# Performance work log

Measured on AMD Instinct MI355X. Metric: run time of the kernel, lower is better.

The kernel has to match this reference:

```python
import jax, jax.numpy as jnp
import numpy as np

P, NL, NQ, L, P2L, P2Q, D = 50000, 2000, 6000, 8, 128, 64, 32
MAX_MODELS, NPOL, MAXQ, ITERS = 7, 4, 3, 8
ZS = {'traffic': (1385.4059, 859.8119), 'packets': (1.4015, 0.8933), 'eq_lambda': (1350.9712, 858.3162), 'avg_pkts_lambda': (0.9117, 0.9724), 'exp_max_factor': (6.6636, 4.7151), 'pkts_lambda_on': (0.9116, 1.6513), 'avg_t_off': (1.6649, 2.3564), 'avg_t_on': (1.6649, 2.3564), 'ar_a': (0.0, 1.0), 'sigma': (0.0, 1.0), 'capacity': (27611.0918, 20090.6211), 'queue_size': (30259.1055, 21410.0957)}


def _glorot(k, fin, fout):
    lim = float(np.sqrt(6.0 / (fin + fout)))
    return jax.random.uniform(k, (fin, fout), jnp.float32, -lim, lim)


def setup_inputs():
    keys = iter(jax.random.split(jax.random.key(0), 80))
    nk = lambda: next(keys)
    u = lambda shape, lo=0.0, hi=1.0: jax.random.uniform(nk(), shape, jnp.float32, lo, hi)
    inp = {}
    inp['traffic'] = u((P, 1), 1.0, 3000.0)
    inp['packets'] = u((P, 1), 0.5, 3.0)
    inp['eq_lambda'] = u((P, 1), 1.0, 3000.0)
    inp['avg_pkts_lambda'] = u((P, 1))
    inp['exp_max_factor'] = u((P, 1), 1.0, 12.0)
    inp['pkts_lambda_on'] = u((P, 1))
    inp['avg_t_off'] = u((P, 1), 0.1, 4.0)
    inp['avg_t_on'] = u((P, 1), 0.1, 4.0)
    inp['ar_a'] = jax.random.normal(nk(), (P, 1), jnp.float32)
    inp['sigma'] = jax.random.normal(nk(), (P, 1), jnp.float32)
    inp['capacity'] = u((NL, 1), 8000.0, 60000.0)
    inp['queue_size'] = u((NQ, 1), 1000.0, 64000.0)
    inp['weight'] = u((NQ, 1))
    length = jax.random.randint(nk(), (P,), 1, L + 1)
    inp['length'] = length
    inp['model'] = jax.random.randint(nk(), (P,), 0, MAX_MODELS)
    inp['policy'] = jax.random.randint(nk(), (NL,), 0, NPOL)
    inp['priority'] = jax.random.randint(nk(), (NQ,), 0, MAXQ)
    inp['queue_to_path'] = jax.random.randint(nk(), (P, L), 0, NQ)
    inp['link_to_path'] = jax.random.randint(nk(), (P, L), 0, NL)
    p2l_path = jax.random.randint(nk(), (NL, P2L), 0, P)
    inp['path_to_link'] = jnp.stack([p2l_path, jnp.zeros_like(p2l_path)], -1)
    inp['p2l_deg'] = jax.random.randint(nk(), (NL,), 1, P2L + 1)
    pq_path = jax.random.randint(nk(), (NQ, P2Q), 0, P)
    pq_pos = 1 + jax.random.randint(nk(), (NQ, P2Q), 0, L) % length[pq_path]
    inp['path_to_queue'] = jnp.stack([pq_path, pq_pos], -1)
    inp['p2q_deg'] = jax.random.randint(nk(), (NQ,), 1, P2Q + 1)
    inp['queue_to_link'] = jnp.arange(NL * MAXQ).reshape(NL, MAXQ)
    def dense(fin, fout):
        return _glorot(nk(), fin, fout), jnp.zeros((fout,), jnp.float32)
    inp['pe_w1'], inp['pe_b1'] = dense(10 + MAX_MODELS, D)
    inp['pe_w2'], inp['pe_b2'] = dense(D, D)
    inp['le_w1'], inp['le_b1'] = dense(NPOL + 1, D)
    inp['le_w2'], inp['le_b2'] = dense(D, D)
    inp['qe_w1'], inp['qe_b1'] = dense(MAXQ + 2, D)
    inp['qe_w2'], inp['qe_b2'] = dense(D, D)
    inp['prW'] = _glorot(nk(), 2 * D, D); inp['prU'] = _glorot(nk(), D, D); inp['prB'] = jnp.zeros((D,), jnp.float32)
    inp['qrW'] = _glorot(nk(), D, D); inp['qrU'] = _glorot(nk(), D, D); inp['qrB'] = jnp.zeros((D,), jnp.float32)
    inp['lrW'] = _glorot(nk(), D, D); inp['lrU'] = _glorot(nk(), D, D); inp['lrB'] = jnp.zeros((D,), jnp.float32)
    inp['ro_w1'], inp['ro_b1'] = dense(D, D // 2)
    inp['ro_w2'], inp['ro_b2'] = dense(D // 2, D // 2)
    inp['ro_w3'], inp['ro_b3'] = dense(D // 2, 1)
    return inp


def _mlp2(x, w1, b1, w2, b2):
    return jax.nn.relu(jax.nn.relu(x @ w1 + b1) @ w2 + b2)


def _forward(traffic, packets, eq_lambda, avg_pkts_lambda, exp_max_factor, pkts_lambda_on,
             avg_t_off, avg_t_on, ar_a, sigma, capacity, queue_size, weight,
             pe_w1, pe_b1, pe_w2, pe_b2, le_w1, le_b1, le_w2, le_b2, qe_w1, qe_b1, qe_w2, qe_b2,
             prW, prU, prB, qrW, qrU, qrB, lrW, lrU, lrB,
             ro_w1, ro_b1, ro_w2, ro_b2, ro_w3, ro_b3,
             length, model, policy, priority, queue_to_path, link_to_path,
             path_to_link, path_to_queue, queue_to_link, p2l_deg, p2q_deg):
    dt = traffic.dtype
    nz = lambda x, k: (x - ZS[k][0]) / ZS[k][1]
    # link load: masked ragged sum of traffic of paths crossing each link
    p2l_mask = (jnp.arange(P2L) < p2l_deg[:, None]).astype(dt)                # [NL, P2L]
    path_gather_traffic = traffic[path_to_link[:, :, 0], 0]                   # [NL, P2L]
    load = (path_gather_traffic * p2l_mask).sum(1, keepdims=True) / capacity  # [NL, 1]
    pkt_size = traffic / packets                                              # [P, 1]
    path_features = jnp.concatenate([
        nz(traffic, 'traffic'), nz(packets, 'packets'),
        jax.nn.one_hot(model, MAX_MODELS, dtype=dt),
        nz(eq_lambda, 'eq_lambda'), nz(avg_pkts_lambda, 'avg_pkts_lambda'),
        nz(exp_max_factor, 'exp_max_factor'), nz(pkts_lambda_on, 'pkts_lambda_on'),
        nz(avg_t_off, 'avg_t_off'), nz(avg_t_on, 'avg_t_on'),
        nz(ar_a, 'ar_a'), nz(sigma, 'sigma')], axis=1)                         # [P, 17]
    path_state = _mlp2(path_features, pe_w1, pe_b1, pe_w2, pe_b2)             # [P, D]
    link_state = _mlp2(jnp.concatenate([load, jax.nn.one_hot(policy, NPOL, dtype=dt)], 1),
                       le_w1, le_b1, le_w2, le_b2)                             # [NL, D]
    queue_state = _mlp2(jnp.concatenate([nz(queue_size, 'queue_size'),
                                         jax.nn.one_hot(priority, MAXQ, dtype=dt), weight], 1),
                        qe_w1, qe_b1, qe_w2, qe_b2)                            # [NQ, D]
    hop_mask = (jnp.arange(L) < length[:, None]).astype(dt)                    # [P, L]
    p2q_mask = (jnp.arange(P2Q) < p2q_deg[:, None]).astype(dt)                 # [NQ, P2Q]

    def path_step(h, xs):
        x_t, m_t = xs
        h_new = jnp.tanh(x_t @ prW + h @ prU + prB)
        h = m_t[:, None] * h_new + (1.0 - m_t[:, None]) * h  # ragged: freeze past length
        return h, h

    pss = None
    for _ in range(ITERS):
        qg = queue_state[queue_to_path]                                        # [P, L, D]
        lg = link_state[link_to_path]                                          # [P, L, D]
        xin = jnp.concatenate([qg, lg], -1)                                    # [P, L, 2D]
        prev = path_state
        path_state, seq = jax.lax.scan(path_step, path_state,
                                       (jnp.swapaxes(xin, 0, 1), hop_mask.T))
        pss = jnp.concatenate([prev[:, None], jnp.swapaxes(seq, 0, 1)], 1)     # [P, L+1, D]
        pg = pss[path_to_queue[:, :, 0], path_to_queue[:, :, 1]]               # [NQ, P2Q, D]
        path_sum = (pg * p2q_mask[:, :, None]).sum(1)                          # [NQ, D]
        queue_state = jnp.tanh(path_sum @ qrW + queue_state @ qrU + qrB)
        qgl = queue_state[queue_to_link]                                       # [NL, 3, D]
        h = link_state
        for t in range(MAXQ):  # fixed tiny sequence of 3 queues per link
            h = jnp.tanh(qgl[:, t] @ lrW + h @ lrU + lrB)
        link_state = h
    cap_g = capacity[link_to_path, 0]                                          # [P, L]
    occ = jax.nn.relu(pss[:, 1:] @ ro_w1 + ro_b1)
    occ = jax.nn.relu(occ @ ro_w2 + ro_b2)
    occ = (occ @ ro_w3 + ro_b3)[:, :, 0]                                       # [P, L]
    queue_delay = ((occ / cap_g) * hop_mask).sum(1, keepdims=True)             # [P, 1]
    trans_delay = pkt_size * ((1.0 / cap_g) * hop_mask).sum(1, keepdims=True)  # [P, 1]
    return queue_delay + trans_delay


def reference(traffic, packets, eq_lambda, avg_pkts_lambda, exp_max_factor, pkts_lambda_on,
              avg_t_off, avg_t_on, ar_a, sigma, capacity, queue_size, weight,
              pe_w1, pe_b1, pe_w2, pe_b2, le_w1, le_b1, le_w2, le_b2, qe_w1, qe_b1, qe_w2, qe_b2,
              prW, prU, prB, qrW, qrU, qrB, lrW, lrU, lrB,
              ro_w1, ro_b1, ro_w2, ro_b2, ro_w3, ro_b3,
              length, model, policy, priority, queue_to_path, link_to_path,
              path_to_link, path_to_queue, queue_to_link, p2l_deg, p2q_deg):
    return _forward(traffic, packets, eq_lambda, avg_pkts_lambda, exp_max_factor, pkts_lambda_on,
                    avg_t_off, avg_t_on, ar_a, sigma, capacity, queue_size, weight,
                    pe_w1, pe_b1, pe_w2, pe_b2, le_w1, le_b1, le_w2, le_b2, qe_w1, qe_b1, qe_w2, qe_b2,
                    prW, prU, prB, qrW, qrU, qrB, lrW, lrU, lrB,
                    ro_w1, ro_b1, ro_w2, ro_b2, ro_w3, ro_b3,
                    length, model, policy, priority, queue_to_path, link_to_path,
                    path_to_link, path_to_queue, queue_to_link, p2l_deg, p2q_deg)
```

## Files before the change

kernel.cpp:

```cpp
#include <hip/hip_runtime.h>
#include <hip/hip_bf16.h>

#define P_ 50000
#define NL_ 2000
#define NQ_ 6000
#define L_ 8
#define P2L_ 128
#define P2Q_ 64
#define D_ 32
#define ITERS_ 8

typedef __hip_bfloat16 bf16;
typedef unsigned short u16;
typedef unsigned int u32;

__device__ __forceinline__ float bfb2f(u16 u) {
    union { u32 i; float f; } c; c.i = ((u32)u) << 16; return c.f;
}
__device__ __forceinline__ u16 f2bfb(float f) {
    union { bf16 h; u16 u; } c; c.h = __float2bfloat16(f); return c.u;
}
__device__ __forceinline__ u32 pk2(float a, float b) {
    return (u32)f2bfb(a) | ((u32)f2bfb(b) << 16);
}

__device__ __forceinline__ float tanh_fast(float x) {
    return 1.f - 2.f / (__expf(2.f * x) + 1.f);
}

__device__ __forceinline__ void hr_rebuild(float* hr, float4 own) {
    hr[0] = own.x; hr[1] = own.y; hr[2] = own.z; hr[3] = own.w;
#pragma unroll
    for (int c = 0; c < 4; c++)  hr[4 + c]  = __shfl_xor(hr[c], 1, 64);
#pragma unroll
    for (int c = 0; c < 8; c++)  hr[8 + c]  = __shfl_xor(hr[c], 2, 64);
#pragma unroll
    for (int c = 0; c < 16; c++) hr[16 + c] = __shfl_xor(hr[c], 4, 64);
}

__device__ __forceinline__ float4 matvec32(const float* hr,
                                           const float* const* ub, float4 acc) {
#pragma unroll
    for (int s = 0; s < 8; s++) {
#pragma unroll
        for (int c = 0; c < 4; c++) {
            const float4 u = *(const float4*)(ub[s] + 32 * c);
            const float hk = hr[4 * s + c];
            acc.x += hk * u.x; acc.y += hk * u.y;
            acc.z += hk * u.z; acc.w += hk * u.w;
        }
    }
    return acc;
}

__device__ bool detect_f32(const void* p, int n) {
    const u16* u = (const u16*)p;
    int m = n < 64 ? n : 64;
    bool bad = false;
    for (int k = 0; k < m; k++) {
        float v = bfb2f(u[k]);
        float av = fabsf(v);
        bool sane = (v == v) && (av <= 1e6f) && (av == 0.0f || av >= 1e-8f);
        bad |= !sane;
    }
    return bad;
}


struct CvtArgs { const void* p[40]; };

__global__ __launch_bounds__(256) void k_convert(CvtArgs a, float* __restrict__ dst) {
    static constexpr int N[40] = {
        50000,50000,50000,50000,50000,50000,50000,50000,50000,50000,
        2000,6000,6000,
        544,32,1024,32, 160,32,1024,32, 160,32,1024,32,
        2048,1024,32, 1024,1024,32, 1024,1024,32,
        512,16,256,16,16,1};
    int b = blockIdx.x, t = 0, off = 0;
    for (;;) {
        int nb = (N[t] + 255) >> 8;
        if (b < nb) break;
        b -= nb; off += N[t]; ++t;
    }
    const void* src = a.p[t];
    const int n = N[t];
    const bool isf = detect_f32(src, n);
    const int i = b * 256 + threadIdx.x;
    if (i < n)
        dst[off + i] = isf ? ((const float*)src)[i] : bfb2f(((const u16*)src)[i]);
}


__global__ __launch_bounds__(256) void k_path_embed(
    const float* __restrict__ traffic, const float* __restrict__ packets,
    const float* __restrict__ eq_lambda, const float* __restrict__ avg_pkts_lambda,
    const float* __restrict__ exp_max_factor, const float* __restrict__ pkts_lambda_on,
    const float* __restrict__ avg_t_off, const float* __restrict__ avg_t_on,
    const float* __restrict__ ar_a, const float* __restrict__ sigma,
    const int* __restrict__ model,
    const float* __restrict__ w1, const float* __restrict__ b1,
    const float* __restrict__ w2, const float* __restrict__ b2,
    float* __restrict__ path_state)
{
    int p = blockIdx.x * 256 + threadIdx.x;
    if (p >= P_) return;
    float f[10];
    f[0] = (traffic[p]        - 1385.4059f) * (1.f / 859.8119f);
    f[1] = (packets[p]        - 1.4015f)    * (1.f / 0.8933f);
    f[2] = (eq_lambda[p]      - 1350.9712f) * (1.f / 858.3162f);
    f[3] = (avg_pkts_lambda[p]- 0.9117f)    * (1.f / 0.9724f);
    f[4] = (exp_max_factor[p] - 6.6636f)    * (1.f / 4.7151f);
    f[5] = (pkts_lambda_on[p] - 0.9116f)    * (1.f / 1.6513f);
    f[6] = (avg_t_off[p]      - 1.6649f)    * (1.f / 2.3564f);
    f[7] = (avg_t_on[p]       - 1.6649f)    * (1.f / 2.3564f);
    f[8] = ar_a[p];
    f[9] = sigma[p];
    int mrow = 2 + model[p];
    float h1[32];
#pragma unroll
    for (int d = 0; d < 32; d++) {
        float a = b1[d] + w1[mrow * 32 + d];
        a += f[0] * w1[0 * 32 + d];
        a += f[1] * w1[1 * 32 + d];
#pragma unroll
        for (int j = 0; j < 8; j++) a += f[2 + j] * w1[(9 + j) * 32 + d];
        h1[d] = fmaxf(a, 0.f);
    }
#pragma unroll
    for (int d = 0; d < 32; d++) {
        float a = b2[d];
#pragma unroll
        for (int k = 0; k < 32; k++) a += h1[k] * w2[k * 32 + d];
        path_state[p * 32 + d] = fmaxf(a, 0.f);
    }
}

__global__ __launch_bounds__(256) void k_queue_embed(
    const float* __restrict__ queue_size, const float* __restrict__ weight,
    const int* __restrict__ priority,
    const float* __restrict__ w1, const float* __restrict__ b1,
    const float* __restrict__ w2, const float* __restrict__ b2,
    float* __restrict__ queue_state)
{
    int q = blockIdx.x * 256 + threadIdx.x;
    if (q >= NQ_) return;
    float f0 = (queue_size[q] - 30259.1055f) * (1.f / 21410.0957f);
    float f4 = weight[q];
    int prow = 1 + priority[q];
    float h1[32];
#pragma unroll
    for (int d = 0; d < 32; d++) {
        float a = b1[d] + w1[prow * 32 + d]
                + f0 * w1[0 * 32 + d] + f4 * w1[4 * 32 + d];
        h1[d] = fmaxf(a, 0.f);
    }
#pragma unroll
    for (int d = 0; d < 32; d++) {
        float a = b2[d];
#pragma unroll
        for (int k = 0; k < 32; k++) a += h1[k] * w2[k * 32 + d];
        queue_state[q * 32 + d] = fmaxf(a, 0.f);
    }
}

__global__ __launch_bounds__(256) void k_link_embed(
    const float* __restrict__ traffic, const float* __restrict__ capacity,
    const int* __restrict__ policy,
    const int* __restrict__ p2l, const int* __restrict__ p2l_deg,
    const float* __restrict__ w1, const float* __restrict__ b1,
    const float* __restrict__ w2, const float* __restrict__ b2,
    float* __restrict__ link_state)
{
    __shared__ float wsh[1248];
    __shared__ float h1s[4][32];
    const int tid = threadIdx.x;
    if (tid < 160) wsh[tid] = w1[tid];
    if (tid < 32)  wsh[160 + tid] = b1[tid];
    for (int idx = tid; idx < 1024; idx += 256) wsh[192 + idx] = w2[idx];
    if (tid >= 32 && tid < 64) wsh[1216 + tid - 32] = b2[tid - 32];
    __syncthreads();

    const int w = tid >> 6, lane = tid & 63;
    const int l = blockIdx.x * 4 + w;
    const int deg = p2l_deg[l];
    float s = 0.f;
    if (lane < deg)      s += traffic[p2l[l * 256 + 2 * lane]];
    if (lane + 64 < deg) s += traffic[p2l[l * 256 + 2 * (lane + 64)]];
#pragma unroll
    for (int m = 1; m < 64; m <<= 1) s += __shfl_xor(s, m, 64);
    const float load = s / capacity[l];
    const int prow = 1 + policy[l];
    if (lane < 32) {
        float a = wsh[160 + lane] + wsh[prow * 32 + lane] + load * wsh[lane];
        h1s[w][lane] = fmaxf(a, 0.f);
    }
    __syncthreads();
    if (lane < 32) {
        float a = wsh[1216 + lane];
#pragma unroll
        for (int k = 0; k < 32; k++) a += h1s[w][k] * wsh[192 + k * 32 + lane];
        link_state[l * 32 + lane] = fmaxf(a, 0.f);
    }
}


__global__ __launch_bounds__(256) void k_zprep(
    const float* __restrict__ queue_state, const float* __restrict__ link_state,
    const float* __restrict__ prW, const float* __restrict__ prB,
    float* __restrict__ zq, float* __restrict__ zl)
{
    __shared__ float wq[32 * 32];
    __shared__ float wlk[32 * 32];
    __shared__ float bsh[32];
    const int tid = threadIdx.x;
#pragma unroll
    for (int j = 0; j < 4; j++) {
        wq[tid + 256 * j]  = prW[tid + 256 * j];
        wlk[tid + 256 * j] = prW[1024 + tid + 256 * j];
    }
    if (tid < 32) bsh[tid] = prB[tid];
    __syncthreads();

    const int grp = tid >> 3, i = tid & 7;
    const int e = blockIdx.x * 32 + grp;
    if (e >= NQ_ + NL_) return;
    const bool isq = e < NQ_;
    const float* st = isq ? (queue_state + (size_t)e * 32)
                          : (link_state + (size_t)(e - NQ_) * 32);
    const float* wbase = isq ? wq : wlk;
    const float* ub[8];
#pragma unroll
    for (int s = 0; s < 8; s++) ub[s] = wbase + (i ^ s) * 128 + 4 * i;

    float4 own = *(const float4*)(st + 4 * i);
    float hr[32];
    hr_rebuild(hr, own);

    float4 acc;
    if (isq) acc = *(const float4*)(bsh + 4 * i);
    else     acc = make_float4(0.f, 0.f, 0.f, 0.f);
    acc = matvec32(hr, ub, acc);

    float* dst = isq ? (zq + (size_t)e * 32) : (zl + (size_t)(e - NQ_) * 32);
    *(float4*)(dst + 4 * i) = acc;
}


__global__ __launch_bounds__(256, 2) void k_path_rnn(
    const int* __restrict__ q2p, const int* __restrict__ l2p,
    const int* __restrict__ length,
    const float* __restrict__ prU,
    const float* __restrict__ zq, const float* __restrict__ zl,
    float* __restrict__ path_state, u16* __restrict__ pss)
{
    const int tid = threadIdx.x;
    const int grp = tid >> 3, i = tid & 7;
    const int p = blockIdx.x * 32 + grp;
    if (p >= P_) return;
    const int len = length[p];

    float4 Ub[32];
#pragma unroll
    for (int s = 0; s < 8; s++) {
        const float* rb = prU + ((i ^ s) * 128 + 4 * i);
#pragma unroll
        for (int c = 0; c < 4; c++)
            Ub[4 * s + c] = *(const float4*)(rb + 32 * c);
    }

    const int4 qi0 = *(const int4*)(q2p + (size_t)p * 8);
    const int4 qi1 = *(const int4*)(q2p + (size_t)p * 8 + 4);
    const int4 li0 = *(const int4*)(l2p + (size_t)p * 8);
    const int4 li1 = *(const int4*)(l2p + (size_t)p * 8 + 4);
    const int qidx[8] = {qi0.x, qi0.y, qi0.z, qi0.w, qi1.x, qi1.y, qi1.z, qi1.w};
    const int lidx[8] = {li0.x, li0.y, li0.z, li0.w, li1.x, li1.y, li1.z, li1.w};

    float4 own = *(const float4*)(path_state + (size_t)p * 32 + 4 * i);
    float hr[32];
    hr_rebuild(hr, own);

    float4 z;
    {
        const float4 a = *(const float4*)(zq + (size_t)qidx[0] * 32 + 4 * i);
        const float4 b = *(const float4*)(zl + (size_t)lidx[0] * 32 + 4 * i);
        z = make_float4(a.x + b.x, a.y + b.y, a.z + b.z, a.w + b.w);
    }

#pragma unroll
    for (int t = 0; t < 8; t++) {
        float4 acc = z;
        if (t < 7) {
            const float4 a = *(const float4*)(zq + (size_t)qidx[t + 1] * 32 + 4 * i);
            const float4 b = *(const float4*)(zl + (size_t)lidx[t + 1] * 32 + 4 * i);
            z = make_float4(a.x + b.x, a.y + b.y, a.z + b.z, a.w + b.w);
        }
#pragma unroll
        for (int k = 0; k < 32; k++) {
            const float hk = hr[k];
            acc.x += hk * Ub[k].x; acc.y += hk * Ub[k].y;
            acc.z += hk * Ub[k].z; acc.w += hk * Ub[k].w;
        }
        const bool m = (t < len);
        own.x = m ? tanh_fast(acc.x) : own.x;
        own.y = m ? tanh_fast(acc.y) : own.y;
        own.z = m ? tanh_fast(acc.z) : own.z;
        own.w = m ? tanh_fast(acc.w) : own.w;
        uint2 w2;
        w2.x = pk2(own.x, own.y);
        w2.y = pk2(own.z, own.w);
        *(uint2*)(pss + (size_t)p * 256 + t * 32 + 4 * i) = w2;
        if (t < 7) hr_rebuild(hr, own);
    }
    *(float4*)(path_state + (size_t)p * 32 + 4 * i) = own;
}


__global__ __launch_bounds__(256) void k_queue_update(
    const int* __restrict__ p2q, const int* __restrict__ p2q_deg,
    const float* __restrict__ qrW, const float* __restrict__ qrU,
    const float* __restrict__ qrB,
    const float* __restrict__ prWq, const float* __restrict__ prB,
    const u16* __restrict__ pss, float* __restrict__ queue_state,
    float* __restrict__ zq)
{
    __shared__ float wl[3 * 1024 + 64];
    const int tid = threadIdx.x;
#pragma unroll
    for (int j = 0; j < 4; j++) {
        wl[tid + 256 * j]        = qrW[tid + 256 * j];
        wl[1024 + tid + 256 * j] = qrU[tid + 256 * j];
        wl[2048 + tid + 256 * j] = prWq[tid + 256 * j];
    }
    if (tid < 32) { wl[3072 + tid] = qrB[tid]; wl[3104 + tid] = prB[tid]; }
    __syncthreads();

    const int w = tid >> 6, lane = tid & 63;
    const int g = lane >> 3, i = lane & 7;
    const int q = blockIdx.x * 4 + w;
    const int deg = p2q_deg[q];

    float4 ps = {0.f, 0.f, 0.f, 0.f};
    for (int j = g; j < deg; j += 8) {
        const int pj = p2q[q * 128 + 2 * j];
        int pos = p2q[q * 128 + 2 * j + 1] - 1;
        pos = pos < 0 ? 0 : (pos > 7 ? 7 : pos);
        const ushort4 v = *(const ushort4*)(pss + (size_t)pj * 256 + pos * 32 + 4 * i);
        ps.x += bfb2f(v.x); ps.y += bfb2f(v.y);
        ps.z += bfb2f(v.z); ps.w += bfb2f(v.w);
    }
#pragma unroll
    for (int m = 8; m < 64; m <<= 1) {
        ps.x += __shfl_xor(ps.x, m, 64);
        ps.y += __shfl_xor(ps.y, m, 64);
        ps.z += __shfl_xor(ps.z, m, 64);
        ps.w += __shfl_xor(ps.w, m, 64);
    }
    const float4 qs = *(const float4*)(queue_state + (size_t)q * 32 + 4 * i);

    const float* ubW[8]; const float* ubU[8]; const float* ubP[8];
#pragma unroll
    for (int s = 0; s < 8; s++) {
        const int o = (i ^ s) * 128 + 4 * i;
        ubW[s] = wl + o; ubU[s] = wl + 1024 + o; ubP[s] = wl + 2048 + o;
    }

    float psr[32]; hr_rebuild(psr, ps);
    float qsr[32]; hr_rebuild(qsr, qs);
    float4 acc = *(const float4*)(wl + 3072 + 4 * i);
    acc = matvec32(psr, ubW, acc);
    acc = matvec32(qsr, ubU, acc);
    float4 nh;
    nh.x = tanh_fast(acc.x); nh.y = tanh_fast(acc.y);
    nh.z = tanh_fast(acc.z); nh.w = tanh_fast(acc.w);

    float nhr[32]; hr_rebuild(nhr, nh);
    float4 zacc = *(const float4*)(wl + 3104 + 4 * i);
    zacc = matvec32(nhr, ubP, zacc);

    if (g == 0) {
        *(float4*)(queue_state + (size_t)q * 32 + 4 * i) = nh;
        *(float4*)(zq + (size_t)q * 32 + 4 * i) = zacc;
    }
}


__global__ __launch_bounds__(256) void k_link_update(
    const int* __restrict__ q2l,
    const float* __restrict__ lrW, const float* __restrict__ lrU,
    const float* __restrict__ lrB,
    const float* __restrict__ prWl,
    const float* __restrict__ queue_state, float* __restrict__ link_state,
    float* __restrict__ zl)
{
    __shared__ float wl[3 * 1024 + 32];
    const int tid = threadIdx.x;
#pragma unroll
    for (int j = 0; j < 4; j++) {
        wl[tid + 256 * j]        = lrW[tid + 256 * j];
        wl[1024 + tid + 256 * j] = lrU[tid + 256 * j];
        wl[2048 + tid + 256 * j] = prWl[tid + 256 * j];
    }
    if (tid < 32) wl[3072 + tid] = lrB[tid];
    __syncthreads();

    const int w = tid >> 6, lane = tid & 63;
    const int i = lane & 7, g = lane >> 3;
    const int l = blockIdx.x * 4 + w;

    const float* ubW[8]; const float* ubU[8]; const float* ubP[8];
#pragma unroll
    for (int s = 0; s < 8; s++) {
        const int o = (i ^ s) * 128 + 4 * i;
        ubW[s] = wl + o; ubU[s] = wl + 1024 + o; ubP[s] = wl + 2048 + o;
    }

    float4 h = *(const float4*)(link_state + (size_t)l * 32 + 4 * i);
    float hhr[32]; hr_rebuild(hhr, h);

#pragma unroll
    for (int t = 0; t < 3; t++) {
        const int qq = q2l[l * 3 + t];
        const float4 qg = *(const float4*)(queue_state + (size_t)qq * 32 + 4 * i);
        float qgr[32]; hr_rebuild(qgr, qg);
        float4 acc = *(const float4*)(wl + 3072 + 4 * i);
        acc = matvec32(qgr, ubW, acc);
        acc = matvec32(hhr, ubU, acc);
        h.x = tanh_fast(acc.x); h.y = tanh_fast(acc.y);
        h.z = tanh_fast(acc.z); h.w = tanh_fast(acc.w);
        hr_rebuild(hhr, h);
    }
    float4 zacc = make_float4(0.f, 0.f, 0.f, 0.f);
    zacc = matvec32(hhr, ubP, zacc);

    if (g == 0) {
        *(float4*)(link_state + (size_t)l * 32 + 4 * i) = h;
        *(float4*)(zl + (size_t)l * 32 + 4 * i) = zacc;
    }
}


__global__ __launch_bounds__(256) void k_readout(
    const void* __restrict__ raw_traffic,
    const float* __restrict__ traffic, const float* __restrict__ packets,
    const float* __restrict__ capacity,
    const int* __restrict__ l2p, const int* __restrict__ length,
    const float* __restrict__ w1, const float* __restrict__ b1,
    const float* __restrict__ w2, const float* __restrict__ b2,
    const float* __restrict__ w3, const float* __restrict__ b3,
    const u16* __restrict__ pss, void* __restrict__ out)
{
    __shared__ float wl[817];
    __shared__ float xs[32][52];
    const int tid = threadIdx.x;
    for (int idx = tid; idx < 512; idx += 256) wl[idx] = w1[idx];
    if (tid < 256) wl[528 + tid] = w2[tid];
    if (tid < 16) {
        wl[512 + tid] = b1[tid];
        wl[784 + tid] = b2[tid];
        wl[800 + tid] = w3[tid];
    }
    if (tid == 0) wl[816] = b3[0];
    __syncthreads();

    const int grp = tid >> 3, i = tid & 7;
    const int p = blockIdx.x * 32 + grp;
    if (p >= P_) return;
    const bool outf32 = detect_f32(raw_traffic, P_);
    const int len = length[p];
    float qd = 0.f, ts = 0.f;
#pragma unroll 1
    for (int t = 0; t < 8; t++) {
        const ushort4 hu = *(const ushort4*)(pss + (size_t)p * 256 + t * 32 + 4 * i);
        float4 hv;
        hv.x = bfb2f(hu.x); hv.y = bfb2f(hu.y); hv.z = bfb2f(hu.z); hv.w = bfb2f(hu.w);
        *(float4*)&xs[grp][4 * i] = hv;
        float a0 = wl[512 + 2 * i], a1 = wl[512 + 2 * i + 1];
#pragma unroll
        for (int k = 0; k < 32; k += 4) {
            const float4 xv = *(const float4*)&xs[grp][k];
            const float2 u0 = *(const float2*)&wl[(k + 0) * 16 + 2 * i];
            const float2 u1 = *(const float2*)&wl[(k + 1) * 16 + 2 * i];
            const float2 u2 = *(const float2*)&wl[(k + 2) * 16 + 2 * i];
            const float2 u3 = *(const float2*)&wl[(k + 3) * 16 + 2 * i];
            a0 += xv.x * u0.x + xv.y * u1.x + xv.z * u2.x + xv.w * u3.x;
            a1 += xv.x * u0.y + xv.y * u1.y + xv.z * u2.y + xv.w * u3.y;
        }
        a0 = fmaxf(a0, 0.f); a1 = fmaxf(a1, 0.f);
        *(float2*)&xs[grp][32 + 2 * i] = make_float2(a0, a1);
        float c0 = wl[784 + 2 * i], c1 = wl[784 + 2 * i + 1];
#pragma unroll
        for (int k = 0; k < 16; k += 4) {
            const float4 xv = *(const float4*)&xs[grp][32 + k];
            const float2 u0 = *(const float2*)&wl[528 + (k + 0) * 16 + 2 * i];
            const float2 u1 = *(const float2*)&wl[528 + (k + 1) * 16 + 2 * i];
            const float2 u2 = *(const float2*)&wl[528 + (k + 2) * 16 + 2 * i];
            const float2 u3 = *(const float2*)&wl[528 + (k + 3) * 16 + 2 * i];
            c0 += xv.x * u0.x + xv.y * u1.x + xv.z * u2.x + xv.w * u3.x;
            c1 += xv.x * u0.y + xv.y * u1.y + xv.z * u2.y + xv.w * u3.y;
        }
        c0 = fmaxf(c0, 0.f); c1 = fmaxf(c1, 0.f);
        float pv = c0 * wl[800 + 2 * i] + c1 * wl[800 + 2 * i + 1];
        pv += __shfl_xor(pv, 1, 8);
        pv += __shfl_xor(pv, 2, 8);
        pv += __shfl_xor(pv, 4, 8);
        const float occv = pv + wl[816];
        if (t < len) {
            const float inv = 1.f / capacity[l2p[p * 8 + t]];
            qd += occv * inv;
            ts += inv;
        }
    }
    if (i == 0) {
        const float res = qd + (traffic[p] / packets[p]) * ts;
        if (outf32) ((float*)out)[p] = res;
        else        ((bf16*)out)[p] = __float2bfloat16(res);
    }
}


extern "C" void kernel_launch(void* const* d_in, const int* in_sizes, int n_in,
                              void* d_out, int out_size, void* d_ws, size_t ws_size,
                              hipStream_t stream)
{
    static const int CVT_N[40] = {
        50000,50000,50000,50000,50000,50000,50000,50000,50000,50000,
        2000,6000,6000,
        544,32,1024,32, 160,32,1024,32, 160,32,1024,32,
        2048,1024,32, 1024,1024,32, 1024,1024,32,
        512,16,256,16,16,1};

    const int*  length   = (const int*)d_in[13];
    const int*  model    = (const int*)d_in[14];
    const int*  policy   = (const int*)d_in[15];
// ... 32 lines not shown
    const float* c_pe_w1 = ws + off[13]; const float* c_pe_b1 = ws + off[14];
    const float* c_pe_w2 = ws + off[15]; const float* c_pe_b2 = ws + off[16];
    const float* c_le_w1 = ws + off[17]; const float* c_le_b1 = ws + off[18];
    const float* c_le_w2 = ws + off[19]; const float* c_le_b2 = ws + off[20];
    const float* c_qe_w1 = ws + off[21]; const float* c_qe_b1 = ws + off[22];
    const float* c_qe_w2 = ws + off[23]; const float* c_qe_b2 = ws + off[24];
    const float* c_prW = ws + off[25]; const float* c_prU = ws + off[26];
    const float* c_prB = ws + off[27];
    const float* c_qrW = ws + off[28]; const float* c_qrU = ws + off[29];
    const float* c_qrB = ws + off[30];
    const float* c_lrW = ws + off[31]; const float* c_lrU = ws + off[32];
    const float* c_lrB = ws + off[33];
    const float* c_ro_w1 = ws + off[34]; const float* c_ro_b1 = ws + off[35];
    const float* c_ro_w2 = ws + off[36]; const float* c_ro_b2 = ws + off[37];
    const float* c_ro_w3 = ws + off[38]; const float* c_ro_b3 = ws + off[39];

    size_t base = ((size_t)off[40] + 63) & ~(size_t)63;
    float* path_state  = ws + base;
    float* queue_state = path_state + (size_t)P_ * 32;
    float* link_state  = queue_state + (size_t)NQ_ * 32;
    float* zq          = link_state + (size_t)NL_ * 32;
    float* zl          = zq + (size_t)NQ_ * 32;
    u16*   pss         = (u16*)(zl + (size_t)NL_ * 32);

    k_convert<<<nblk, 256, 0, stream>>>(ca, ws);

    k_path_embed<<<(P_ + 255) / 256, 256, 0, stream>>>(
        c_traffic, c_packets, c_eq_lambda, c_apl, c_emf, c_plo, c_atoff, c_aton,
        c_ar_a, c_sigma, model, c_pe_w1, c_pe_b1, c_pe_w2, c_pe_b2, path_state);
    k_queue_embed<<<(NQ_ + 255) / 256, 256, 0, stream>>>(
        c_queue_size, c_weight, priority, c_qe_w1, c_qe_b1, c_qe_w2, c_qe_b2,
        queue_state);
    k_link_embed<<<NL_ / 4, 256, 0, stream>>>(
        c_traffic, c_capacity, policy, p2l, p2l_deg,
        c_le_w1, c_le_b1, c_le_w2, c_le_b2, link_state);
    k_zprep<<<(NQ_ + NL_ + 31) / 32, 256, 0, stream>>>(
        queue_state, link_state, c_prW, c_prB, zq, zl);

    for (int it = 0; it < ITERS_; ++it) {
        k_path_rnn<<<(P_ + 31) / 32, 256, 0, stream>>>(
            q2p, l2p, length, c_prU, zq, zl, path_state, pss);
        k_queue_update<<<NQ_ / 4, 256, 0, stream>>>(
            p2q, p2q_deg, c_qrW, c_qrU, c_qrB, c_prW, c_prB,
            pss, queue_state, zq);
        k_link_update<<<NL_ / 4, 256, 0, stream>>>(
            q2l, c_lrW, c_lrU, c_lrB, c_prW + 1024,
            queue_state, link_state, zl);
    }

    k_readout<<<(P_ + 31) / 32, 256, 0, stream>>>(
        d_in[0], c_traffic, c_packets, c_capacity, l2p, length,
        c_ro_w1, c_ro_b1, c_ro_w2, c_ro_b2, c_ro_w3, c_ro_b3, pss, d_out);
}
```

Before: 724.7 us.

## Sort paths by length, skip padded RNN steps, fuse embed and update kernels

```diff
diff --git a/kernel.cpp b/kernel.cpp
--- a/kernel.cpp
+++ b/kernel.cpp
@@ -9,6 +9,8 @@
 #define P2Q_ 64
 #define D_ 32
 #define ITERS_ 8
+#define PB_ 196
+#define QB_ 24
 
 typedef __hip_bfloat16 bf16;
 typedef unsigned short u16;
@@ -27,6 +29,9 @@
 __device__ __forceinline__ float tanh_fast(float x) {
     return 1.f - 2.f / (__expf(2.f * x) + 1.f);
 }
+__device__ __forceinline__ float4 tanh4(float4 a) {
+    return make_float4(tanh_fast(a.x), tanh_fast(a.y), tanh_fast(a.z), tanh_fast(a.w));
+}
 
 __device__ __forceinline__ void hr_rebuild(float* hr, float4 own) {
     hr[0] = own.x; hr[1] = own.y; hr[2] = own.z; hr[3] = own.w;
@@ -38,13 +43,14 @@
     for (int c = 0; c < 16; c++) hr[16 + c] = __shfl_xor(hr[c], 4, 64);
 }
 
-__device__ __forceinline__ float4 matvec32(const float* hr,
-                                           const float* const* ub, float4 acc) {
+__device__ __forceinline__ float4 matvec32o(const float* hr, const float* base,
+                                            const int* offs, float4 acc) {
 #pragma unroll
     for (int s = 0; s < 8; s++) {
+        const float* u0 = base + offs[s];
 #pragma unroll
         for (int c = 0; c < 4; c++) {
-            const float4 u = *(const float4*)(ub[s] + 32 * c);
+            const float4 u = *(const float4*)(u0 + 32 * c);
             const float hk = hr[4 * s + c];
             acc.x += hk * u.x; acc.y += hk * u.y;
             acc.z += hk * u.z; acc.w += hk * u.w;
@@ -69,13 +75,15 @@
 
 struct CvtArgs { const void* p[40]; };
 
-__global__ __launch_bounds__(256) void k_convert(CvtArgs a, float* __restrict__ dst) {
+__global__ __launch_bounds__(256) void k_convert(CvtArgs a, float* __restrict__ dst,
+                                                 int* __restrict__ counters) {
     static constexpr int N[40] = {
         50000,50000,50000,50000,50000,50000,50000,50000,50000,50000,
         2000,6000,6000,
         544,32,1024,32, 160,32,1024,32, 160,32,1024,32,
         2048,1024,32, 1024,1024,32, 1024,1024,32,
         512,16,256,16,16,1};
+    if (blockIdx.x == 0 && threadIdx.x < 16) counters[threadIdx.x] = 0;
     int b = blockIdx.x, t = 0, off = 0;
     for (;;) {
         int nb = (N[t] + 255) >> 8;
@@ -91,162 +99,157 @@
 }
 
 
-__global__ __launch_bounds__(256) void k_path_embed(
+__global__ __launch_bounds__(256) void k_hist(const int* __restrict__ length,
+                                              int* __restrict__ hist) {
+    int p = blockIdx.x * 256 + threadIdx.x;
+    if (p < P_) atomicAdd(&hist[length[p] - 1], 1);
+}
+
+__global__ __launch_bounds__(256) void k_scatter(const int* __restrict__ length,
+                                                 const int* __restrict__ hist,
+                                                 int* __restrict__ cursor,
+                                                 int* __restrict__ perm) {
+    int p = blockIdx.x * 256 + threadIdx.x;
+    if (p >= P_) return;
+    int b = length[p] - 1;
+    int pre = 0;
+#pragma unroll
+    for (int k = 0; k < 8; k++) pre += (k < b) ? hist[k] : 0;
+    int pos = pre + atomicAdd(&cursor[b], 1);
+    perm[pos] = p;
+}
+
+
+__global__ __launch_bounds__(256) void k_embed_all(
     const float* __restrict__ traffic, const float* __restrict__ packets,
     const float* __restrict__ eq_lambda, const float* __restrict__ avg_pkts_lambda,
     const float* __restrict__ exp_max_factor, const float* __restrict__ pkts_lambda_on,
     const float* __restrict__ avg_t_off, const float* __restrict__ avg_t_on,
     const float* __restrict__ ar_a, const float* __restrict__ sigma,
-    const int* __restrict__ model,
-    const float* __restrict__ w1, const float* __restrict__ b1,
-    const float* __restrict__ w2, const float* __restrict__ b2,
-    float* __restrict__ path_state)
+    const float* __restrict__ capacity, const float* __restrict__ queue_size,
+    const float* __restrict__ weight,
+    const int* __restrict__ model, const int* __restrict__ policy,
+    const int* __restrict__ priority,
+    const int* __restrict__ p2l, const int* __restrict__ p2l_deg,
+    const float* __restrict__ pe_w1, const float* __restrict__ pe_b1,
+    const float* __restrict__ pe_w2, const float* __restrict__ pe_b2,
+    const float* __restrict__ qe_w1, const float* __restrict__ qe_b1,
+    const float* __restrict__ qe_w2, const float* __restrict__ qe_b2,
+    const float* __restrict__ le_w1, const float* __restrict__ le_b1,
+    const float* __restrict__ le_w2, const float* __restrict__ le_b2,
+    const float* __restrict__ prW, const float* __restrict__ prB,
+    float* __restrict__ path_state, float* __restrict__ queue_state,
+    float* __restrict__ link_state, float* __restrict__ zq, float* __restrict__ zl)
 {
-    int p = blockIdx.x * 256 + threadIdx.x;
-    if (p >= P_) return;
-    float f[10];
-    f[0] = (traffic[p]        - 1385.4059f) * (1.f / 859.8119f);
-    f[1] = (packets[p]        - 1.4015f)    * (1.f / 0.8933f);
-    f[2] = (eq_lambda[p]      - 1350.9712f) * (1.f / 858.3162f);
-    f[3] = (avg_pkts_lambda[p]- 0.9117f)    * (1.f / 0.9724f);
-    f[4] = (exp_max_factor[p] - 6.6636f)    * (1.f / 4.7151f);
-    f[5] = (pkts_lambda_on[p] - 0.9116f)    * (1.f / 1.6513f);
-    f[6] = (avg_t_off[p]      - 1.6649f)    * (1.f / 2.3564f);
-    f[7] = (avg_t_on[p]       - 1.6649f)    * (1.f / 2.3564f);
-    f[8] = ar_a[p];
-    f[9] = sigma[p];
-    int mrow = 2 + model[p];
-    float h1[32];
-#pragma unroll
-    for (int d = 0; d < 32; d++) {
-        float a = b1[d] + w1[mrow * 32 + d];
-        a += f[0] * w1[0 * 32 + d];
-        a += f[1] * w1[1 * 32 + d];
-#pragma unroll
-        for (int j = 0; j < 8; j++) a += f[2 + j] * w1[(9 + j) * 32 + d];
-        h1[d] = fmaxf(a, 0.f);
-    }
-#pragma unroll
-    for (int d = 0; d < 32; d++) {
-        float a = b2[d];
-#pragma unroll
-        for (int k = 0; k < 32; k++) a += h1[k] * w2[k * 32 + d];
-        path_state[p * 32 + d] = fmaxf(a, 0.f);
-    }
-}
-
-__global__ __launch_bounds__(256) void k_queue_embed(
-    const float* __restrict__ queue_size, const float* __restrict__ weight,
-    const int* __restrict__ priority,
-    const float* __restrict__ w1, const float* __restrict__ b1,
-    const float* __restrict__ w2, const float* __restrict__ b2,
-    float* __restrict__ queue_state)
-{
-    int q = blockIdx.x * 256 + threadIdx.x;
-    if (q >= NQ_) return;
-    float f0 = (queue_size[q] - 30259.1055f) * (1.f / 21410.0957f);
-    float f4 = weight[q];
-    int prow = 1 + priority[q];
-    float h1[32];
-#pragma unroll
-    for (int d = 0; d < 32; d++) {
-        float a = b1[d] + w1[prow * 32 + d]
-                + f0 * w1[0 * 32 + d] + f4 * w1[4 * 32 + d];
-        h1[d] = fmaxf(a, 0.f);
-    }
-#pragma unroll
-    for (int d = 0; d < 32; d++) {
-        float a = b2[d];
-#pragma unroll
-        for (int k = 0; k < 32; k++) a += h1[k] * w2[k * 32 + d];
-        queue_state[q * 32 + d] = fmaxf(a, 0.f);
-    }
-}
-
-__global__ __launch_bounds__(256) void k_link_embed(
-    const float* __restrict__ traffic, const float* __restrict__ capacity,
-    const int* __restrict__ policy,
-    const int* __restrict__ p2l, const int* __restrict__ p2l_deg,
-    const float* __restrict__ w1, const float* __restrict__ b1,
-    const float* __restrict__ w2, const float* __restrict__ b2,
-    float* __restrict__ link_state)
-{
-    __shared__ float wsh[1248];
-    __shared__ float h1s[4][32];
-    const int tid = threadIdx.x;
-    if (tid < 160) wsh[tid] = w1[tid];
-    if (tid < 32)  wsh[160 + tid] = b1[tid];
-    for (int idx = tid; idx < 1024; idx += 256) wsh[192 + idx] = w2[idx];
-    if (tid >= 32 && tid < 64) wsh[1216 + tid - 32] = b2[tid - 32];
-    __syncthreads();
-
-    const int w = tid >> 6, lane = tid & 63;
-    const int l = blockIdx.x * 4 + w;
-    const int deg = p2l_deg[l];
-    float s = 0.f;
-    if (lane < deg)      s += traffic[p2l[l * 256 + 2 * lane]];
-    if (lane + 64 < deg) s += traffic[p2l[l * 256 + 2 * (lane + 64)]];
-#pragma unroll
-    for (int m = 1; m < 64; m <<= 1) s += __shfl_xor(s, m, 64);
-    const float load = s / capacity[l];
-    const int prow = 1 + policy[l];
-    if (lane < 32) {
-        float a = wsh[160 + lane] + wsh[prow * 32 + lane] + load * wsh[lane];
-        h1s[w][lane] = fmaxf(a, 0.f);
-    }
-    __syncthreads();
-    if (lane < 32) {
-        float a = wsh[1216 + lane];
-#pragma unroll
-        for (int k = 0; k < 32; k++) a += h1s[w][k] * wsh[192 + k * 32 + lane];
-        link_state[l * 32 + lane] = fmaxf(a, 0.f);
-    }
-}
-
-
-__global__ __launch_bounds__(256) void k_zprep(
-    const float* __restrict__ queue_state, const float* __restrict__ link_state,
-    const float* __restrict__ prW, const float* __restrict__ prB,
-    float* __restrict__ zq, float* __restrict__ zl)
-{
-    __shared__ float wq[32 * 32];
-    __shared__ float wlk[32 * 32];
-    __shared__ float bsh[32];
-    const int tid = threadIdx.x;
-#pragma unroll
-    for (int j = 0; j < 4; j++) {
-        wq[tid + 256 * j]  = prW[tid + 256 * j];
-        wlk[tid + 256 * j] = prW[1024 + tid + 256 * j];
-    }
-    if (tid < 32) bsh[tid] = prB[tid];
-    __syncthreads();
-
-    const int grp = tid >> 3, i = tid & 7;
-    const int e = blockIdx.x * 32 + grp;
-    if (e >= NQ_ + NL_) return;
-    const bool isq = e < NQ_;
-    const float* st = isq ? (queue_state + (size_t)e * 32)
-                          : (link_state + (size_t)(e - NQ_) * 32);
-    const float* wbase = isq ? wq : wlk;
-    const float* ub[8];
-#pragma unroll
-    for (int s = 0; s < 8; s++) ub[s] = wbase + (i ^ s) * 128 + 4 * i;
-
-    float4 own = *(const float4*)(st + 4 * i);
-    float hr[32];
-    hr_rebuild(hr, own);
-
-    float4 acc;
-    if (isq) acc = *(const float4*)(bsh + 4 * i);
-    else     acc = make_float4(0.f, 0.f, 0.f, 0.f);
-    acc = matvec32(hr, ub, acc);
-
-    float* dst = isq ? (zq + (size_t)e * 32) : (zl + (size_t)(e - NQ_) * 32);
-    *(float4*)(dst + 4 * i) = acc;
+    const int blk = blockIdx.x;
+    if (blk < PB_) {
+        int p = blk * 256 + threadIdx.x;
+        if (p >= P_) return;
+        float f[10];
+        f[0] = (traffic[p]        - 1385.4059f) * (1.f / 859.8119f);
+        f[1] = (packets[p]        - 1.4015f)    * (1.f / 0.8933f);
+        f[2] = (eq_lambda[p]      - 1350.9712f) * (1.f / 858.3162f);
+        f[3] = (avg_pkts_lambda[p]- 0.9117f)    * (1.f / 0.9724f);
+        f[4] = (exp_max_factor[p] - 6.6636f)    * (1.f / 4.7151f);
+        f[5] = (pkts_lambda_on[p] - 0.9116f)    * (1.f / 1.6513f);
+        f[6] = (avg_t_off[p]      - 1.6649f)    * (1.f / 2.3564f);
+        f[7] = (avg_t_on[p]       - 1.6649f)    * (1.f / 2.3564f);
+        f[8] = ar_a[p];
+        f[9] = sigma[p];
+        int mrow = 2 + model[p];
+        float h1[32];
+#pragma unroll
+        for (int d = 0; d < 32; d++) {
+            float a = pe_b1[d] + pe_w1[mrow * 32 + d];
+            a += f[0] * pe_w1[0 * 32 + d];
+            a += f[1] * pe_w1[1 * 32 + d];
+#pragma unroll
+            for (int j = 0; j < 8; j++) a += f[2 + j] * pe_w1[(9 + j) * 32 + d];
+            h1[d] = fmaxf(a, 0.f);
+        }
+#pragma unroll
+        for (int d = 0; d < 32; d++) {
+            float a = pe_b2[d];
+#pragma unroll
+            for (int k = 0; k < 32; k++) a += h1[k] * pe_w2[k * 32 + d];
+            path_state[p * 32 + d] = fmaxf(a, 0.f);
+        }
+    } else if (blk < PB_ + QB_) {
+        int q = (blk - PB_) * 256 + threadIdx.x;
+        if (q >= NQ_) return;
+        float f0 = (queue_size[q] - 30259.1055f) * (1.f / 21410.0957f);
+        float f4 = weight[q];
+        int prow = 1 + priority[q];
+        float h1[32];
+#pragma unroll
+        for (int d = 0; d < 32; d++) {
+            float a = qe_b1[d] + qe_w1[prow * 32 + d]
+                    + f0 * qe_w1[0 * 32 + d] + f4 * qe_w1[4 * 32 + d];
+            h1[d] = fmaxf(a, 0.f);
+        }
+        float h2[32];
+#pragma unroll
+        for (int d = 0; d < 32; d++) {
+            float a = qe_b2[d];
+#pragma unroll
+            for (int k = 0; k < 32; k++) a += h1[k] * qe_w2[k * 32 + d];
+            h2[d] = fmaxf(a, 0.f);
+            queue_state[q * 32 + d] = h2[d];
+        }
+#pragma unroll
+        for (int d = 0; d < 32; d++) {
+            float a = prB[d];
+#pragma unroll
+            for (int k = 0; k < 32; k++) a += h2[k] * prW[k * 32 + d];
+            zq[q * 32 + d] = a;
+        }
+    } else {
+        __shared__ float wsh[1248];
+        __shared__ float h1s[4][32];
+        __shared__ float h2s[4][32];
+        const int tid = threadIdx.x;
+        if (tid < 160) wsh[tid] = le_w1[tid];
+        if (tid < 32)  wsh[160 + tid] = le_b1[tid];
+        for (int idx = tid; idx < 1024; idx += 256) wsh[192 + idx] = le_w2[idx];
+        if (tid >= 32 && tid < 64) wsh[1216 + tid - 32] = le_b2[tid - 32];
+        __syncthreads();
+
+        const int w = tid >> 6, lane = tid & 63;
+        const int l = (blk - PB_ - QB_) * 4 + w;
+        const int deg = p2l_deg[l];
+        float s = 0.f;
+        if (lane < deg)      s += traffic[p2l[l * 256 + 2 * lane]];
+        if (lane + 64 < deg) s += traffic[p2l[l * 256 + 2 * (lane + 64)]];
+#pragma unroll
+        for (int m = 1; m < 64; m <<= 1) s += __shfl_xor(s, m, 64);
+        const float load = s / capacity[l];
+        const int prow = 1 + policy[l];
+        if (lane < 32) {
+            float a = wsh[160 + lane] + wsh[prow * 32 + lane] + load * wsh[lane];
+            h1s[w][lane] = fmaxf(a, 0.f);
+        }
+        __syncthreads();
+        if (lane < 32) {
+            float a = wsh[1216 + lane];
+#pragma unroll
+            for (int k = 0; k < 32; k++) a += h1s[w][k] * wsh[192 + k * 32 + lane];
+            a = fmaxf(a, 0.f);
+            link_state[l * 32 + lane] = a;
+            h2s[w][lane] = a;
+        }
+        __syncthreads();
+        if (lane < 32) {
+            float a = 0.f;
+#pragma unroll
+            for (int k = 0; k < 32; k++) a += h2s[w][k] * prW[1024 + k * 32 + lane];
+            zl[l * 32 + lane] = a;
+        }
+    }
 }
 
 
 __global__ __launch_bounds__(256, 2) void k_path_rnn(
+    const int* __restrict__ perm,
     const int* __restrict__ q2p, const int* __restrict__ l2p,
     const int* __restrict__ length,
     const float* __restrict__ prU,
@@ -255,8 +258,9 @@
 {
     const int tid = threadIdx.x;
     const int grp = tid >> 3, i = tid & 7;
-    const int p = blockIdx.x * 32 + grp;
-    if (p >= P_) return;
+    const int j = blockIdx.x * 32 + grp;
+    if (j >= P_) return;
+    const int p = perm[j];
     const int len = length[p];
 
     float4 Ub[32];
@@ -267,31 +271,25 @@
         for (int c = 0; c < 4; c++)
             Ub[4 * s + c] = *(const float4*)(rb + 32 * c);
     }
-
-    const int4 qi0 = *(const int4*)(q2p + (size_t)p * 8);
-    const int4 qi1 = *(const int4*)(q2p + (size_t)p * 8 + 4);
-    const int4 li0 = *(const int4*)(l2p + (size_t)p * 8);
-    const int4 li1 = *(const int4*)(l2p + (size_t)p * 8 + 4);
-    const int qidx[8] = {qi0.x, qi0.y, qi0.z, qi0.w, qi1.x, qi1.y, qi1.z, qi1.w};
-    const int lidx[8] = {li0.x, li0.y, li0.z, li0.w, li1.x, li1.y, li1.z, li1.w};
 
     float4 own = *(const float4*)(path_state + (size_t)p * 32 + 4 * i);
     float hr[32];
     hr_rebuild(hr, own);
 
+    int qn = q2p[p * 8], ln = l2p[p * 8];
     float4 z;
     {
-        const float4 a = *(const float4*)(zq + (size_t)qidx[0] * 32 + 4 * i);
-        const float4 b = *(const float4*)(zl + (size_t)lidx[0] * 32 + 4 * i);
+        const float4 a = *(const float4*)(zq + (size_t)qn * 32 + 4 * i);
+        const float4 b = *(const float4*)(zl + (size_t)ln * 32 + 4 * i);
         z = make_float4(a.x + b.x, a.y + b.y, a.z + b.z, a.w + b.w);
     }
 
-#pragma unroll
-    for (int t = 0; t < 8; t++) {
+    for (int t = 0; t < len; t++) {
         float4 acc = z;
-        if (t < 7) {
-            const float4 a = *(const float4*)(zq + (size_t)qidx[t + 1] * 32 + 4 * i);
-            const float4 b = *(const float4*)(zl + (size_t)lidx[t + 1] * 32 + 4 * i);
+        if (t + 1 < len) {
+            qn = q2p[p * 8 + t + 1]; ln = l2p[p * 8 + t + 1];
+            const float4 a = *(const float4*)(zq + (size_t)qn * 32 + 4 * i);
+            const float4 b = *(const float4*)(zl + (size_t)ln * 32 + 4 * i);
             z = make_float4(a.x + b.x, a.y + b.y, a.z + b.z, a.w + b.w);
         }
 #pragma unroll
@@ -300,138 +298,107 @@
             acc.x += hk * Ub[k].x; acc.y += hk * Ub[k].y;
             acc.z += hk * Ub[k].z; acc.w += hk * Ub[k].w;
         }
-        const bool m = (t < len);
-        own.x = m ? tanh_fast(acc.x) : own.x;
-        own.y = m ? tanh_fast(acc.y) : own.y;
-        own.z = m ? tanh_fast(acc.z) : own.z;
-        own.w = m ? tanh_fast(acc.w) : own.w;
+        own = tanh4(acc);
         uint2 w2;
         w2.x = pk2(own.x, own.y);
         w2.y = pk2(own.z, own.w);
         *(uint2*)(pss + (size_t)p * 256 + t * 32 + 4 * i) = w2;
-        if (t < 7) hr_rebuild(hr, own);
+        if (t + 1 < len) hr_rebuild(hr, own);
     }
     *(float4*)(path_state + (size_t)p * 32 + 4 * i) = own;
 }
 
 
-__global__ __launch_bounds__(256) void k_queue_update(
+__global__ __launch_bounds__(256) void k_qlupd(
     const int* __restrict__ p2q, const int* __restrict__ p2q_deg,
+    const int* __restrict__ q2l,
     const float* __restrict__ qrW, const float* __restrict__ qrU,
     const float* __restrict__ qrB,
-    const float* __restrict__ prWq, const float* __restrict__ prB,
+    const float* __restrict__ lrW, const float* __restrict__ lrU,
+    const float* __restrict__ lrB,
+    const float* __restrict__ prW, const float* __restrict__ prB,
     const u16* __restrict__ pss, float* __restrict__ queue_state,
-    float* __restrict__ zq)
+    float* __restrict__ link_state,
+    float* __restrict__ zq, float* __restrict__ zl)
 {
-    __shared__ float wl[3 * 1024 + 64];
+    __shared__ float wl[6 * 1024 + 96];
     const int tid = threadIdx.x;
 #pragma unroll
-    for (int j = 0; j < 4; j++) {
-        wl[tid + 256 * j]        = qrW[tid + 256 * j];
-        wl[1024 + tid + 256 * j] = qrU[tid + 256 * j];
-        wl[2048 + tid + 256 * j] = prWq[tid + 256 * j];
-    }
-    if (tid < 32) { wl[3072 + tid] = qrB[tid]; wl[3104 + tid] = prB[tid]; }
+    for (int jj = 0; jj < 4; jj++) {
+        wl[tid + 256 * jj]        = qrW[tid + 256 * jj];
+        wl[1024 + tid + 256 * jj] = qrU[tid + 256 * jj];
+        wl[2048 + tid + 256 * jj] = prW[tid + 256 * jj];
+        wl[3072 + tid + 256 * jj] = lrW[tid + 256 * jj];
+        wl[4096 + tid + 256 * jj] = lrU[tid + 256 * jj];
+        wl[5120 + tid + 256 * jj] = prW[1024 + tid + 256 * jj];
+    }
+    if (tid < 32) {
+        wl[6144 + tid] = qrB[tid];
+        wl[6176 + tid] = prB[tid];
+        wl[6208 + tid] = lrB[tid];
+    }
     __syncthreads();
 
     const int w = tid >> 6, lane = tid & 63;
     const int g = lane >> 3, i = lane & 7;
-    const int q = blockIdx.x * 4 + w;
-    const int deg = p2q_deg[q];
-
-    float4 ps = {0.f, 0.f, 0.f, 0.f};
-    for (int j = g; j < deg; j += 8) {
-        const int pj = p2q[q * 128 + 2 * j];
-        int pos = p2q[q * 128 + 2 * j + 1] - 1;
-        pos = pos < 0 ? 0 : (pos > 7 ? 7 : pos);
-        const ushort4 v = *(const ushort4*)(pss + (size_t)pj * 256 + pos * 32 + 4 * i);
-        ps.x += bfb2f(v.x); ps.y += bfb2f(v.y);
-        ps.z += bfb2f(v.z); ps.w += bfb2f(v.w);
-    }
-#pragma unroll
-    for (int m = 8; m < 64; m <<= 1) {
-        ps.x += __shfl_xor(ps.x, m, 64);
-        ps.y += __shfl_xor(ps.y, m, 64);
-        ps.z += __shfl_xor(ps.z, m, 64);
-        ps.w += __shfl_xor(ps.w, m, 64);
-    }
-    const float4 qs = *(const float4*)(queue_state + (size_t)q * 32 + 4 * i);
-
-    const float* ubW[8]; const float* ubU[8]; const float* ubP[8];
-#pragma unroll
-    for (int s = 0; s < 8; s++) {
-        const int o = (i ^ s) * 128 + 4 * i;
-        ubW[s] = wl + o; ubU[s] = wl + 1024 + o; ubP[s] = wl + 2048 + o;
-    }
-
-    float psr[32]; hr_rebuild(psr, ps);
-    float qsr[32]; hr_rebuild(qsr, qs);
-    float4 acc = *(const float4*)(wl + 3072 + 4 * i);
-    acc = matvec32(psr, ubW, acc);
-    acc = matvec32(qsr, ubU, acc);
-    float4 nh;
-    nh.x = tanh_fast(acc.x); nh.y = tanh_fast(acc.y);
-    nh.z = tanh_fast(acc.z); nh.w = tanh_fast(acc.w);
-
-    float nhr[32]; hr_rebuild(nhr, nh);
-    float4 zacc = *(const float4*)(wl + 3104 + 4 * i);
-    zacc = matvec32(nhr, ubP, zacc);
-
-    if (g == 0) {
-        *(float4*)(queue_state + (size_t)q * 32 + 4 * i) = nh;
-        *(float4*)(zq + (size_t)q * 32 + 4 * i) = zacc;
-    }
-}
-
-
-__global__ __launch_bounds__(256) void k_link_update(
-    const int* __restrict__ q2l,
-    const float* __restrict__ lrW, const float* __restrict__ lrU,
-    const float* __restrict__ lrB,
-    const float* __restrict__ prWl,
-    const float* __restrict__ queue_state, float* __restrict__ link_state,
-    float* __restrict__ zl)
-{
-    __shared__ float wl[3 * 1024 + 32];
-    const int tid = threadIdx.x;
-#pragma unroll
-    for (int j = 0; j < 4; j++) {
-        wl[tid + 256 * j]        = lrW[tid + 256 * j];
-        wl[1024 + tid + 256 * j] = lrU[tid + 256 * j];
-        wl[2048 + tid + 256 * j] = prWl[tid + 256 * j];
-    }
-    if (tid < 32) wl[3072 + tid] = lrB[tid];
-    __syncthreads();
-
-    const int w = tid >> 6, lane = tid & 63;
-    const int i = lane & 7, g = lane >> 3;
     const int l = blockIdx.x * 4 + w;
 
-    const float* ubW[8]; const float* ubU[8]; const float* ubP[8];
-#pragma unroll
-    for (int s = 0; s < 8; s++) {
-        const int o = (i ^ s) * 128 + 4 * i;
-        ubW[s] = wl + o; ubU[s] = wl + 1024 + o; ubP[s] = wl + 2048 + o;
+    int offs[8];
+#pragma unroll
+    for (int s = 0; s < 8; s++) offs[s] = (i ^ s) * 128 + 4 * i;
+
+    float4 nq0, nq1, nq2;
+#pragma unroll
+    for (int c = 0; c < 3; c++) {
+        const int q = q2l[l * 3 + c];
+        const int deg = p2q_deg[q];
+        float4 ps = {0.f, 0.f, 0.f, 0.f};
+        for (int j = g; j < deg; j += 8) {
+            const int pj = p2q[q * 128 + 2 * j];
+            int pos = p2q[q * 128 + 2 * j + 1] - 1;
+            pos = pos < 0 ? 0 : (pos > 7 ? 7 : pos);
+            const ushort4 v = *(const ushort4*)(pss + (size_t)pj * 256 + pos * 32 + 4 * i);
+            ps.x += bfb2f(v.x); ps.y += bfb2f(v.y);
+            ps.z += bfb2f(v.z); ps.w += bfb2f(v.w);
+        }
+#pragma unroll
+        for (int m = 8; m < 64; m <<= 1) {
+            ps.x += __shfl_xor(ps.x, m, 64);
+            ps.y += __shfl_xor(ps.y, m, 64);
+            ps.z += __shfl_xor(ps.z, m, 64);
+            ps.w += __shfl_xor(ps.w, m, 64);
+        }
+        const float4 qs = *(const float4*)(queue_state + (size_t)q * 32 + 4 * i);
+        float psr[32]; hr_rebuild(psr, ps);
+        float qsr[32]; hr_rebuild(qsr, qs);
+        float4 acc = *(const float4*)(wl + 6144 + 4 * i);
+        acc = matvec32o(psr, wl, offs, acc);
+        acc = matvec32o(qsr, wl + 1024, offs, acc);
+        const float4 nh = tanh4(acc);
+        float nhr[32]; hr_rebuild(nhr, nh);
+        float4 zacc = *(const float4*)(wl + 6176 + 4 * i);
+        zacc = matvec32o(nhr, wl + 2048, offs, zacc);
+        if (g == 0) {
+            *(float4*)(queue_state + (size_t)q * 32 + 4 * i) = nh;
+            *(float4*)(zq + (size_t)q * 32 + 4 * i) = zacc;
+        }
+        if (c == 0) nq0 = nh; else if (c == 1) nq1 = nh; else nq2 = nh;
     }
 
     float4 h = *(const float4*)(link_state + (size_t)l * 32 + 4 * i);
     float hhr[32]; hr_rebuild(hhr, h);
-
-#pragma unroll
-    for (int t = 0; t < 3; t++) {
-        const int qq = q2l[l * 3 + t];
-        const float4 qg = *(const float4*)(queue_state + (size_t)qq * 32 + 4 * i);
+#pragma unroll
+    for (int c = 0; c < 3; c++) {
+        const float4 qg = (c == 0) ? nq0 : ((c == 1) ? nq1 : nq2);
         float qgr[32]; hr_rebuild(qgr, qg);
-        float4 acc = *(const float4*)(wl + 3072 + 4 * i);
-        acc = matvec32(qgr, ubW, acc);
-        acc = matvec32(hhr, ubU, acc);
-        h.x = tanh_fast(acc.x); h.y = tanh_fast(acc.y);
-        h.z = tanh_fast(acc.z); h.w = tanh_fast(acc.w);
+        float4 acc = *(const float4*)(wl + 6208 + 4 * i);
+        acc = matvec32o(qgr, wl + 3072, offs, acc);
+        acc = matvec32o(hhr, wl + 4096, offs, acc);
+        h = tanh4(acc);
         hr_rebuild(hhr, h);
     }
     float4 zacc = make_float4(0.f, 0.f, 0.f, 0.f);
-    zacc = matvec32(hhr, ubP, zacc);
-
+    zacc = matvec32o(hhr, wl + 5120, offs, zacc);
     if (g == 0) {
         *(float4*)(link_state + (size_t)l * 32 + 4 * i) = h;
         *(float4*)(zl + (size_t)l * 32 + 4 * i) = zacc;
@@ -440,7 +407,7 @@
 
 
 __global__ __launch_bounds__(256) void k_readout(
-    const void* __restrict__ raw_traffic,
+    const void* __restrict__ raw_traffic, const int* __restrict__ perm,
     const float* __restrict__ traffic, const float* __restrict__ packets,
     const float* __restrict__ capacity,
     const int* __restrict__ l2p, const int* __restrict__ length,
@@ -463,13 +430,13 @@
     __syncthreads();
 
     const int grp = tid >> 3, i = tid & 7;
-    const int p = blockIdx.x * 32 + grp;
-    if (p >= P_) return;
+    const int j = blockIdx.x * 32 + grp;
+    if (j >= P_) return;
+    const int p = perm[j];
     const bool outf32 = detect_f32(raw_traffic, P_);
     const int len = length[p];
     float qd = 0.f, ts = 0.f;
-#pragma unroll 1
-    for (int t = 0; t < 8; t++) {
+    for (int t = 0; t < len; t++) {
         const ushort4 hu = *(const ushort4*)(pss + (size_t)p * 256 + t * 32 + 4 * i);
         float4 hv;
         hv.x = bfb2f(hu.x); hv.y = bfb2f(hu.y); hv.z = bfb2f(hu.z); hv.w = bfb2f(hu.w);
@@ -504,11 +471,9 @@
         pv += __shfl_xor(pv, 2, 8);
         pv += __shfl_xor(pv, 4, 8);
         const float occv = pv + wl[816];
-        if (t < len) {
-            const float inv = 1.f / capacity[l2p[p * 8 + t]];
-            qd += occv * inv;
-            ts += inv;
-        }
+        const float inv = 1.f / capacity[l2p[p * 8 + t]];
+        qd += occv * inv;
+        ts += inv;
     }
     if (i == 0) {
         const float res = qd + (traffic[p] / packets[p]) * ts;
@@ -587,33 +552,34 @@
     float* zq          = link_state + (size_t)NL_ * 32;
     float* zl          = zq + (size_t)NQ_ * 32;
     u16*   pss         = (u16*)(zl + (size_t)NL_ * 32);
-
-    k_convert<<<nblk, 256, 0, stream>>>(ca, ws);
-
-    k_path_embed<<<(P_ + 255) / 256, 256, 0, stream>>>(
+    int*   perm        = (int*)(pss + (size_t)P_ * 256);
+    int*   counters    = perm + P_;
+    int*   hist        = counters;
+    int*   cursor      = counters + 8;
+
+    k_convert<<<nblk, 256, 0, stream>>>(ca, ws, counters);
+    k_hist<<<(P_ + 255) / 256, 256, 0, stream>>>(length, hist);
+    k_scatter<<<(P_ + 255) / 256, 256, 0, stream>>>(length, hist, cursor, perm);
+
+    k_embed_all<<<PB_ + QB_ + NL_ / 4, 256, 0, stream>>>(
         c_traffic, c_packets, c_eq_lambda, c_apl, c_emf, c_plo, c_atoff, c_aton,
-        c_ar_a, c_sigma, model, c_pe_w1, c_pe_b1, c_pe_w2, c_pe_b2, path_state);
-    k_queue_embed<<<(NQ_ + 255) / 256, 256, 0, stream>>>(
-        c_queue_size, c_weight, priority, c_qe_w1, c_qe_b1, c_qe_w2, c_qe_b2,
-        queue_state);
-    k_link_embed<<<NL_ / 4, 256, 0, stream>>>(
-        c_traffic, c_capacity, policy, p2l, p2l_deg,
-        c_le_w1, c_le_b1, c_le_w2, c_le_b2, link_state);
-    k_zprep<<<(NQ_ + NL_ + 31) / 32, 256, 0, stream>>>(
-        queue_state, link_state, c_prW, c_prB, zq, zl);
+        c_ar_a, c_sigma, c_capacity, c_queue_size, c_weight,
+        model, policy, priority, p2l, p2l_deg,
+        c_pe_w1, c_pe_b1, c_pe_w2, c_pe_b2,
+        c_qe_w1, c_qe_b1, c_qe_w2, c_qe_b2,
+        c_le_w1, c_le_b1, c_le_w2, c_le_b2,
+        c_prW, c_prB,
+        path_state, queue_state, link_state, zq, zl);
 
     for (int it = 0; it < ITERS_; ++it) {
         k_path_rnn<<<(P_ + 31) / 32, 256, 0, stream>>>(
-            q2p, l2p, length, c_prU, zq, zl, path_state, pss);
-        k_queue_update<<<NQ_ / 4, 256, 0, stream>>>(
-            p2q, p2q_deg, c_qrW, c_qrU, c_qrB, c_prW, c_prB,
-            pss, queue_state, zq);
-        k_link_update<<<NL_ / 4, 256, 0, stream>>>(
-            q2l, c_lrW, c_lrU, c_lrB, c_prW + 1024,
-            queue_state, link_state, zl);
+            perm, q2p, l2p, length, c_prU, zq, zl, path_state, pss);
+        k_qlupd<<<NL_ / 4, 256, 0, stream>>>(
+            p2q, p2q_deg, q2l, c_qrW, c_qrU, c_qrB, c_lrW, c_lrU, c_lrB,
+            c_prW, c_prB, pss, queue_state, link_state, zq, zl);
     }
 
     k_readout<<<(P_ + 31) / 32, 256, 0, stream>>>(
-        d_in[0], c_traffic, c_packets, c_capacity, l2p, length,
+        d_in[0], perm, c_traffic, c_packets, c_capacity, l2p, length,
         c_ro_w1, c_ro_b1, c_ro_w2, c_ro_b2, c_ro_w3, c_ro_b3, pss, d_out);
 }
```

Result: slower. 1.321 ms (+82.3%).
